# Kernel tuning notes

Hardware: AMD Instinct MI355X
Metric: run time of the kernel (lower is better)

Reference implementation:

```python
import jax, jax.numpy as jnp
import numpy as np

NUM_LAYERS = 3
NODE_DIM = 32
TIME_DIM = 32
N_HEAD = 4
N_NODES = 1_000_000
BATCH = 256
MODEL_DIM = NODE_DIM + TIME_DIM  # 64
HEAD_DIM = MODEL_DIM // N_HEAD   # 16


def setup_inputs() -> dict:
    key = jax.random.key(0)
    ks = jax.random.split(key, 20)
    L, D, F = NUM_LAYERS, MODEL_DIM, NODE_DIM
    s = 0.1
    return {
        "src_idx": jax.random.randint(ks[0], (BATCH,), 0, N_NODES),
        "target_idx": jax.random.randint(ks[1], (BATCH,), 0, N_NODES),
        "cut_time": jax.random.uniform(ks[2], (BATCH,), dtype=jnp.float32) * 10000.0,
        "num_neighbors": 20,
        # learned params
        "emb": jax.random.uniform(ks[3], (N_NODES, F), minval=-1.0, maxval=1.0, dtype=jnp.float32),
        "time_freq": (1.0 / 10.0 ** jnp.linspace(0.0, 9.0, TIME_DIM)).astype(jnp.float32),
        "time_phase": jnp.zeros((TIME_DIM,), jnp.float32),
        "Wq": jax.random.normal(ks[4], (L, D, D), jnp.float32) * s,
        "Wk": jax.random.normal(ks[5], (L, D, D), jnp.float32) * s,
        "Wv": jax.random.normal(ks[6], (L, D, D), jnp.float32) * s,
        "Wo": jax.random.normal(ks[7], (L, D, D), jnp.float32) * s,
        "mw1": jax.random.normal(ks[8], (L, D + F, F), jnp.float32) * s,
        "mb1": jnp.zeros((L, F), jnp.float32),
        "mw2": jax.random.normal(ks[9], (L, F, F), jnp.float32) * s,
        "mb2": jnp.zeros((L, F), jnp.float32),
        "aff_w1": jax.random.normal(ks[10], (2 * F, F), jnp.float32) * s,
        "aff_b1": jnp.zeros((F,), jnp.float32),
        "aff_w2": jax.random.normal(ks[11], (F, 1), jnp.float32) * s,
        "aff_b2": jnp.zeros((1,), jnp.float32),
    }


def _time_encode(ts, freq, phase):
    # ts: [...]; output [..., TIME_DIM] harmonic encoding (TGAT TimeEncode)
    return jnp.cos(ts[..., None] * freq + phase)


def _sample_neighbors(nodes, times, num_neighbors):
    # Deterministic stand-in for ngh_finder.get_temporal_neighbor (CPU sampler).
    j = jnp.arange(num_neighbors)
    ngh = (nodes[:, None] * 101 + (j + 1) * 7919) % N_NODES        # [n, K] int
    frac = (j + 1).astype(times.dtype) / (num_neighbors + 1)
    ngh_t = times[:, None] * frac                                  # earlier timestamps
    return ngh, ngh_t


def _attn_layer(l, src_feat, src_t_emb, ngh_feat, ngh_t_emb, mask, p):
    # TGAT-style AttnModel: MHA over [feat||time_emb], then MergeLayer(attn_out, src_feat)
    n, K = ngh_feat.shape[0], ngh_feat.shape[1]
    q_in = jnp.concatenate([src_feat, src_t_emb], axis=-1)            # [n, D]
    k_in = jnp.concatenate([ngh_feat, ngh_t_emb], axis=-1)           # [n, K, D]
    q = (q_in @ p["Wq"][l]).reshape(n, N_HEAD, HEAD_DIM)
    k = (k_in @ p["Wk"][l]).reshape(n, K, N_HEAD, HEAD_DIM)
    v = (k_in @ p["Wv"][l]).reshape(n, K, N_HEAD, HEAD_DIM)
    scores = jnp.einsum("nhd,nkhd->nhk", q, k) / jnp.sqrt(jnp.float32(HEAD_DIM))
    scores = jnp.where(mask[:, None, :], -1e9, scores)
    attn = jax.nn.softmax(scores, axis=-1)
    out = jnp.einsum("nhk,nkhd->nhd", attn, v).reshape(n, MODEL_DIM) @ p["Wo"][l]
    h = jax.nn.relu(jnp.concatenate([out, src_feat], axis=-1) @ p["mw1"][l] + p["mb1"][l])
    return h @ p["mw2"][l] + p["mb2"][l]                              # [n, F]


def _tem_conv(nodes, times, layer, num_neighbors, p):
    feat = p["emb"][nodes]                                            # gather [n, F]
    if layer == 0:
        return feat
    src_conv = _tem_conv(nodes, times, layer - 1, num_neighbors, p)   # [n, F]
    ngh, ngh_t = _sample_neighbors(nodes, times, num_neighbors)       # [n, K]
    delta = times[:, None] - ngh_t                                    # [n, K]
    n = nodes.shape[0]
    ngh_conv = _tem_conv(ngh.reshape(-1), ngh_t.reshape(-1), layer - 1,
                         num_neighbors, p).reshape(n, num_neighbors, NODE_DIM)
    src_t_emb = _time_encode(jnp.zeros_like(times), p["time_freq"], p["time_phase"])  # [n, T]
    ngh_t_emb = _time_encode(delta, p["time_freq"], p["time_phase"])  # [n, K, T]
    mask = ngh == 0
    return _attn_layer(layer - 1, src_conv, src_t_emb, ngh_conv, ngh_t_emb, mask, p)


def reference(src_idx, target_idx, cut_time, num_neighbors, emb, time_freq, time_phase,
              Wq, Wk, Wv, Wo, mw1, mb1, mw2, mb2, aff_w1, aff_b1, aff_w2, aff_b2):
    p = dict(emb=emb, time_freq=time_freq, time_phase=time_phase, Wq=Wq, Wk=Wk, Wv=Wv,
             Wo=Wo, mw1=mw1, mb1=mb1, mw2=mw2, mb2=mb2)
    src_embed = _tem_conv(src_idx, cut_time, NUM_LAYERS, num_neighbors, p)
    tgt_embed = _tem_conv(target_idx, cut_time, NUM_LAYERS, num_neighbors, p)
    h = jax.nn.relu(jnp.concatenate([src_embed, tgt_embed], axis=-1) @ aff_w1 + aff_b1)
    return (h @ aff_w2 + aff_b2).squeeze(-1)                          # [B]
```

## Files before the change

kernel.cpp:

```cpp
#include <hip/hip_runtime.h>
#include <math.h>

#define K 20
#define KP1 21
#define F 32
#define NNODES 1000000

#define NP1 112896
#define NP2 5376
#define NP3 256

#define WBLK 16640
#define OFF_H1 49920
#define OFF_H2 (OFF_H1 + 2 * NP1 * F)
#define OFF_H3 (OFF_H2 + 2 * NP2 * F)

#define LDS_M4   12544
#define LDS_WAVE 13568
#define WV_STRIDE 3296
#define SMEM_FLOATS (LDS_WAVE + 8 * WV_STRIDE)

__device__ __forceinline__ int nhash(int node, int j) {
    return (node * 101 + (j + 1) * 7919) % NNODES;
}

__global__ __launch_bounds__(256) void transform_weights(
    const float* __restrict__ Wq, const float* __restrict__ Wk,
    const float* __restrict__ Wv, const float* __restrict__ Wo,
    const float* __restrict__ mw1, const float* __restrict__ mw2,
    const float* __restrict__ phase, float* __restrict__ ws)
{
    const int l = blockIdx.x, tid = threadIdx.x;
    const float* wq = Wq + l * 4096; const float* wk = Wk + l * 4096;
    const float* wv = Wv + l * 4096; const float* wo = Wo + l * 4096;
    const float* m1 = mw1 + l * 3072; const float* m2 = mw2 + l * 1024;
    float* out = ws + l * WBLK;
    for (int i = tid; i < 8192; i += 256) {
        const int a = i >> 8, e = (i >> 2) & 63, h = i & 3;
        float s = 0.f;
        for (int t = 0; t < 16; ++t) s += wq[a * 64 + h * 16 + t] * wk[e * 64 + h * 16 + t];
        out[i] = s;
    }
    for (int i = tid; i < 256; i += 256) {
        const int e = i >> 2, h = i & 3;
        float s = 0.f;
        for (int a = 0; a < 32; ++a) {
            float acc = 0.f;
            for (int t = 0; t < 16; ++t) acc += wq[(32 + a) * 64 + h * 16 + t] * wk[e * 64 + h * 16 + t];
            s += cosf(phase[a]) * acc;
        }
        out[8192 + i] = s;
    }
    for (int i = tid; i < 4096; i += 256) {
        const int e4 = i >> 8, d = (i >> 2) & 63, c = i & 3;
        out[8448 + i] = wv[(4 * e4 + c) * 64 + d];
    }
    for (int i = tid; i < 3072; i += 256) {
        const int k4 = i >> 7, f = (i >> 2) & 31, c = i & 3;
        const int k = 4 * k4 + c;
        float v;
        if (k < 64) { v = 0.f; for (int g2 = 0; g2 < 64; ++g2) v += wo[k * 64 + g2] * m1[g2 * 32 + f]; }
        else v = m1[k * 32 + f];
        out[12544 + i] = v;
    }
    for (int i = tid; i < 1024; i += 256) {
        const int e4 = i >> 7, d = (i >> 2) & 31, c = i & 3;
        out[15616 + i] = m2[(4 * e4 + c) * 32 + d];
    }
}

template<int LEVEL>
__global__ __launch_bounds__(512, 2) void attn_kernel(
    const int* __restrict__ src_idx, const int* __restrict__ tgt_idx,
    const float* __restrict__ cut_time, const float* __restrict__ emb,
    const float* __restrict__ freq, const float* __restrict__ phase,
    const float* __restrict__ ws_w,
    const float* __restrict__ mb1_, const float* __restrict__ mb2_,
    const float* __restrict__ h_in, float* __restrict__ h_out)
{
    constexpr int NPAIRS = (LEVEL == 1) ? NP1 : (LEVEL == 2 ? NP2 : NP3);
    constexpr int PREVN  = (LEVEL == 2) ? NP1 : NP2;
    constexpr int l = LEVEL - 1;
    constexpr int NBATCH = NPAIRS;

    extern __shared__ float smem[];

    const int tid  = threadIdx.x;
    const int w    = tid >> 6;
    const int lane = tid & 63;
    const int h    = lane >> 4;
    const int c3   = lane & 7;
    const int rep  = (lane >> 3) & 1;
    const int td   = lane & 31;
    const int half = lane >> 5;

    {
        const float* wsrc = ws_w + l * WBLK;
        for (int i4 = tid; i4 < 3136; i4 += 512)
            *(float4*)&smem[i4 * 4] = *(const float4*)&wsrc[i4 * 4];
        for (int i4 = tid; i4 < 256; i4 += 512)
            *(float4*)&smem[LDS_M4 + i4 * 4] = *(const float4*)&wsrc[15616 + i4 * 4];
    }
    __syncthreads();

    float* sM   = smem;
    float* sC   = smem + 8192;
    float* sWv4 = smem + 8448;
    float* sm4  = smem + LDS_M4;
    float* wb   = smem + LDS_WAVE + w * WV_STRIDE;
    float* kin0 = wb;
    float* kin1 = wb + 1280;
    float* qf0  = wb + 2560;
    float* qf1  = wb + 2592;
    float* qz0  = wb + 2624;
    float* qz1  = wb + 2896;
    float* ob0  = wb + 3168;
    float* ob1  = wb + 3232;

    const float* P4g = ws_w + l * WBLK + 12544;

    const float fr = freq[td], ph = phase[td];
    const float b1v = mb1_[l * 32 + td], b2v = mb2_[l * 32 + td];

    const int gstride = gridDim.x * 8;
    float4 pf[2][3]; int na[2]; float ta[2];

    auto PRE = [&](int bb) {
        #pragma unroll
        for (int q = 0; q < 2; ++q) {
            const int i    = bb * 2 + q;
            const int side = (i >= NPAIRS) ? 1 : 0;
            const int p    = i - side * NPAIRS;
            int b, s2 = 0, r = 0;
            if (LEVEL == 3)      { b = p; }
            else if (LEVEL == 2) { b = p / KP1; s2 = p % KP1; }
            else                 { int qq = p / KP1; r = p % KP1; b = qq / KP1; s2 = qq % KP1; }
            const int root = side ? tgt_idx[b] : src_idx[b];
            const float ct = cut_time[b];
            int nodeA; float tA;
            if (LEVEL == 3) { nodeA = root; tA = ct; }
            else if (LEVEL == 2) {
                nodeA = s2 ? nhash(root, s2 - 1) : root;
                tA    = s2 ? ct * ((float)s2 / 21.0f) : ct;
            } else {
                const int   n2 = s2 ? nhash(root, s2 - 1) : root;
                const float t2 = s2 ? ct * ((float)s2 / 21.0f) : ct;
                nodeA = r ? nhash(n2, r - 1) : n2;
                tA    = r ? t2 * ((float)r / 21.0f) : t2;
            }
            na[q] = nodeA; ta[q] = tA;
            if (LEVEL == 1) {
                { const int row = lane >> 3, c4 = lane & 7;
                  const int node = row ? nhash(nodeA, row - 1) : nodeA;
                  pf[q][0] = *(const float4*)&emb[(size_t)node * F + c4 * 4]; }
                { const int idx4 = 64 + lane, row = idx4 >> 3, c4 = idx4 & 7;
                  const int node = nhash(nodeA, row - 1);
                  pf[q][1] = *(const float4*)&emb[(size_t)node * F + c4 * 4]; }
                { const int idx4 = 128 + lane;
                  if (idx4 < 168) {
                      const int row = idx4 >> 3, c4 = idx4 & 7;
                      const int node = nhash(nodeA, row - 1);
                      pf[q][2] = *(const float4*)&emb[(size_t)node * F + c4 * 4]; } }
            } else {
                const float* base = h_in + ((size_t)side * PREVN + (size_t)p * KP1) * F;
                pf[q][0] = *(const float4*)&base[lane * 4];
                pf[q][1] = *(const float4*)&base[(64 + lane) * 4];
                if (128 + lane < 168) pf[q][2] = *(const float4*)&base[(128 + lane) * 4];
            }
        }
    };

    int g = blockIdx.x * 8 + w;
    if (g < NBATCH) PRE(g);

    for (; g < NBATCH; g += gstride) {
        const int gs = g;
        const int cna0 = na[0], cna1 = na[1];
        const float cta0 = ta[0], cta1 = ta[1];

        #pragma unroll
        for (int q = 0; q < 2; ++q) {
            float* kin = q ? kin1 : kin0;
            float* qfb = q ? qf1 : qf0;
            { const int row = lane >> 3, c4 = lane & 7;
              if (row == 0) *(float4*)&qfb[c4 * 4] = pf[q][0];
              else          *(float4*)&kin[(row - 1) * 64 + c4 * 4] = pf[q][0]; }
            { const int idx4 = 64 + lane, row = idx4 >> 3, c4 = idx4 & 7;
              *(float4*)&kin[(row - 1) * 64 + c4 * 4] = pf[q][1]; }
            { const int idx4 = 128 + lane;
              if (idx4 < 168) { const int row = idx4 >> 3, c4 = idx4 & 7;
                *(float4*)&kin[(row - 1) * 64 + c4 * 4] = pf[q][2]; } }
        }

        #pragma unroll
        for (int it = 0; it < 10; ++it) {
            const int j = it * 2 + half;
            { const float ngh_t = cta0 * ((float)(j + 1) / 21.0f);
              const float delta = cta0 - ngh_t;
              kin0[j * 64 + 32 + td] = cosf(delta * fr + ph); }
            { const float ngh_t = cta1 * ((float)(j + 1) / 21.0f);
              const float delta = cta1 - ngh_t;
              kin1[j * 64 + 32 + td] = cosf(delta * fr + ph); }
        }
        unsigned mb[2];
        { int m = (cna0 * 101 + 7919) % NNODES; unsigned bits = 0;
          #pragma unroll
          for (int j = 0; j < K; ++j) { if (m == 0) bits |= (1u << j); m += 7919; if (m >= NNODES) m -= NNODES; }
          mb[0] = bits; }
        { int m = (cna1 * 101 + 7919) % NNODES; unsigned bits = 0;
          #pragma unroll
          for (int j = 0; j < K; ++j) { if (m == 0) bits |= (1u << j); m += 7919; if (m >= NNODES) m -= NNODES; }
          mb[1] = bits; }

        if (g + gstride < NBATCH) PRE(g + gstride);

        float4 acc0 = *(const float4*)&sC[lane * 4];
        float4 acc1 = acc0;
        #pragma unroll
        for (int a4 = 0; a4 < 8; ++a4) {
            const float4 f0 = *(float4*)&qf0[a4 * 4];
            const float4 f1 = *(float4*)&qf1[a4 * 4];
            const float4 m0 = *(const float4*)&sM[(a4 * 4 + 0) * 256 + lane * 4];
            const float4 m1v = *(const float4*)&sM[(a4 * 4 + 1) * 256 + lane * 4];
            const float4 m2v = *(const float4*)&sM[(a4 * 4 + 2) * 256 + lane * 4];
            const float4 m3 = *(const float4*)&sM[(a4 * 4 + 3) * 256 + lane * 4];
            acc0.x += f0.x * m0.x + f0.y * m1v.x + f0.z * m2v.x + f0.w * m3.x;
            acc0.y += f0.x * m0.y + f0.y * m1v.y + f0.z * m2v.y + f0.w * m3.y;
            acc0.z += f0.x * m0.z + f0.y * m1v.z + f0.z * m2v.z + f0.w * m3.z;
            acc0.w += f0.x * m0.w + f0.y * m1v.w + f0.z * m2v.w + f0.w * m3.w;
            acc1.x += f1.x * m0.x + f1.y * m1v.x + f1.z * m2v.x + f1.w * m3.x;
            acc1.y += f1.x * m0.y + f1.y * m1v.y + f1.z * m2v.y + f1.w * m3.y;
            acc1.z += f1.x * m0.z + f1.y * m1v.z + f1.z * m2v.z + f1.w * m3.z;
            acc1.w += f1.x * m0.w + f1.y * m1v.w + f1.z * m2v.w + f1.w * m3.w;
        }
        qz0[0 * 68 + lane] = acc0.x; qz0[1 * 68 + lane] = acc0.y;
        qz0[2 * 68 + lane] = acc0.z; qz0[3 * 68 + lane] = acc0.w;
        qz1[0 * 68 + lane] = acc1.x; qz1[1 * 68 + lane] = acc1.y;
        qz1[2 * 68 + lane] = acc1.z; qz1[3 * 68 + lane] = acc1.w;

        const int ofsA = c3 * 8 + rep * 4;
        const int ofsB = c3 * 8 + 4 - rep * 4;
        const int j0 = rep * 10;
        #pragma unroll
        for (int q = 0; q < 2; ++q) {
            float* kin = q ? kin1 : kin0;
            float* qzb = q ? qz1 : qz0;
            const float4 qkA = *(float4*)&qzb[h * 68 + ofsA];
            const float4 qkB = *(float4*)&qzb[h * 68 + ofsB];
            float sc[10];
            #pragma unroll
            for (int t = 0; t < 10; ++t) {
                const float4 kA = *(float4*)&kin[(j0 + t) * 64 + ofsA];
                const float4 kB = *(float4*)&kin[(j0 + t) * 64 + ofsB];
                sc[t] = qkA.x * kA.x + qkA.y * kA.y + qkA.z * kA.z + qkA.w * kA.w
                      + qkB.x * kB.x + qkB.y * kB.y + qkB.z * kB.z + qkB.w * kB.w;
            }
            #pragma unroll
            for (int off = 1; off < 8; off <<= 1) {
                #pragma unroll
                for (int t = 0; t < 10; ++t) sc[t] += __shfl_xor(sc[t], off, 8);
            }
            #pragma unroll
            for (int t = 0; t < 10; ++t) {
                float s = sc[t] * 0.25f;
                if ((mb[q] >> (j0 + t)) & 1) s = -1e9f;
                sc[t] = s;
            }
            float mx = sc[0];
            #pragma unroll
            for (int t = 1; t < 10; ++t) mx = fmaxf(mx, sc[t]);
            mx = fmaxf(mx, __shfl_xor(mx, 8, 16));
            float sum = 0.f;
            #pragma unroll
            for (int t = 0; t < 10; ++t) { sc[t] = __expf(sc[t] - mx); sum += sc[t]; }
            sum += __shfl_xor(sum, 8, 16);
            const float inv = 1.0f / sum;
            float4 zA = {0, 0, 0, 0}, zB = {0, 0, 0, 0};
            #pragma unroll
            for (int t = 0; t < 10; ++t) {
                const float4 kA = *(float4*)&kin[(j0 + t) * 64 + ofsA];
                const float4 kB = *(float4*)&kin[(j0 + t) * 64 + ofsB];
                zA.x += sc[t] * kA.x; zA.y += sc[t] * kA.y; zA.z += sc[t] * kA.z; zA.w += sc[t] * kA.w;
                zB.x += sc[t] * kB.x; zB.y += sc[t] * kB.y; zB.z += sc[t] * kB.z; zB.w += sc[t] * kB.w;
            }
            float4 fA, fB;
            fA.x = zA.x + __shfl_xor(zB.x, 8, 16); fA.y = zA.y + __shfl_xor(zB.y, 8, 16);
            fA.z = zA.z + __shfl_xor(zB.z, 8, 16); fA.w = zA.w + __shfl_xor(zB.w, 8, 16);
            fB.x = zB.x + __shfl_xor(zA.x, 8, 16); fB.y = zB.y + __shfl_xor(zA.y, 8, 16);
            fB.z = zB.z + __shfl_xor(zA.z, 8, 16); fB.w = zB.w + __shfl_xor(zA.w, 8, 16);
            fA.x *= inv; fA.y *= inv; fA.z *= inv; fA.w *= inv;
            fB.x *= inv; fB.y *= inv; fB.z *= inv; fB.w *= inv;
            if (rep == 0) {
                *(float4*)&qzb[h * 68 + ofsA] = fA;
                *(float4*)&qzb[h * 68 + ofsB] = fB;
            }
        }

        float od0 = 0.f, od1 = 0.f;
        #pragma unroll
        for (int e4 = 0; e4 < 16; ++e4) {
            const float4 wv = *(float4*)&sWv4[e4 * 256 + lane * 4];
            const float4 z0 = *(float4*)&qz0[h * 68 + e4 * 4];
            const float4 z1 = *(float4*)&qz1[h * 68 + e4 * 4];
            od0 += z0.x * wv.x + z0.y * wv.y + z0.z * wv.z + z0.w * wv.w;
            od1 += z1.x * wv.x + z1.y * wv.y + z1.z * wv.z + z1.w * wv.w;
        }
        ob0[lane] = od0;
        ob1[lane] = od1;

        float hv0 = 0.f, hv1 = 0.f;
        #pragma unroll
        for (int e4 = 0; e4 < 12; ++e4) {
            float4 x0, x1;
            if (half == 0) { x0 = *(float4*)&ob0[e4 * 4]; x1 = *(float4*)&ob1[e4 * 4]; }
            else {
                x0 = (e4 < 4) ? *(float4*)&ob0[48 + e4 * 4] : *(float4*)&qf0[(e4 - 4) * 4];
                x1 = (e4 < 4) ? *(float4*)&ob1[48 + e4 * 4] : *(float4*)&qf1[(e4 - 4) * 4];
            }
            const float4 w4 = *(const float4*)&P4g[(half * 12 + e4) * 128 + td * 4];
            hv0 += x0.x * w4.x + x0.y * w4.y + x0.z * w4.z + x0.w * w4.w;
            hv1 += x1.x * w4.x + x1.y * w4.y + x1.z * w4.z + x1.w * w4.w;
        }
        hv0 += __shfl_xor(hv0, 32);
        hv1 += __shfl_xor(hv1, 32);
        hv0 = fmaxf(hv0 + b1v, 0.0f);
        hv1 = fmaxf(hv1 + b1v, 0.0f);
        if (lane < 32) { ob0[td] = hv0; ob1[td] = hv1; }

        float y0 = 0.f, y1 = 0.f;
        #pragma unroll
        for (int e4 = 0; e4 < 4; ++e4) {
            const float4 w4 = *(float4*)&sm4[(half * 4 + e4) * 128 + td * 4];
            const float4 x0 = *(float4*)&ob0[half * 16 + e4 * 4];
            const float4 x1 = *(float4*)&ob1[half * 16 + e4 * 4];
            y0 += x0.x * w4.x + x0.y * w4.y + x0.z * w4.z + x0.w * w4.w;
            y1 += x1.x * w4.x + x1.y * w4.y + x1.z * w4.z + x1.w * w4.w;
        }
        y0 += __shfl_xor(y0, 32);
        y1 += __shfl_xor(y1, 32);
        if (lane < 32) {
            #pragma unroll
            for (int q = 0; q < 2; ++q) {
                const int i    = gs * 2 + q;
                const int side = (i >= NPAIRS) ? 1 : 0;
                const int p    = i - side * NPAIRS;
                const float y  = (q == 0) ? y0 : y1;
                h_out[((size_t)side * NPAIRS + p) * F + td] = y + b2v;
            }
        }
    }
}

__global__ __launch_bounds__(256) void final_kernel(
    const float* __restrict__ h3,
    const float* __restrict__ aw1, const float* __restrict__ ab1,
    const float* __restrict__ aw2, const float* __restrict__ ab2,
    float* __restrict__ out)
{
    const int bidx = threadIdx.x;
    float x[64];
    #pragma unroll
    for (int e = 0; e < 32; ++e) {
        x[e]      = h3[(size_t)bidx * 32 + e];
        x[32 + e] = h3[((size_t)NP3 + bidx) * 32 + e];
    }
    float acc = ab2[0];
    for (int f = 0; f < 32; ++f) {
        float hv = ab1[f];
        #pragma unroll
        for (int e = 0; e < 64; ++e) hv += x[e] * aw1[e * 32 + f];
        acc += fmaxf(hv, 0.0f) * aw2[f];
    }
    out[bidx] = acc;
}

extern "C" void kernel_launch(void* const* d_in, const int* in_sizes, int n_in,
                              void* d_out, int out_size, void* d_ws, size_t ws_size,
                              hipStream_t stream)
{
    const int*   src_idx = (const int*)d_in[0];
    const int*   tgt_idx = (const int*)d_in[1];
    const float* cut     = (const float*)d_in[2];
    const float* emb   = (const float*)d_in[4];
    const float* freq  = (const float*)d_in[5];
    const float* phase = (const float*)d_in[6];
    const float* Wq    = (const float*)d_in[7];
    const float* Wk    = (const float*)d_in[8];
    const float* Wv    = (const float*)d_in[9];
    const float* Wo    = (const float*)d_in[10];
    const float* mw1   = (const float*)d_in[11];
    const float* mb1   = (const float*)d_in[12];
    const float* mw2   = (const float*)d_in[13];
    const float* mb2   = (const float*)d_in[14];
    const float* aw1   = (const float*)d_in[15];
    const float* ab1   = (const float*)d_in[16];
    const float* aw2   = (const float*)d_in[17];
    const float* ab2   = (const float*)d_in[18];

    float* ws = (float*)d_ws;
    float* h1 = ws + OFF_H1;
    float* h2 = ws + OFF_H2;
    float* h3 = ws + OFF_H3;

    const size_t smem_bytes = SMEM_FLOATS * sizeof(float);
    hipFuncSetAttribute((const void*)attn_kernel<1>, hipFuncAttributeMaxDynamicSharedMemorySize, (int)smem_bytes);
    hipFuncSetAttribute((const void*)attn_kernel<2>, hipFuncAttributeMaxDynamicSharedMemorySize, (int)smem_bytes);
    hipFuncSetAttribute((const void*)attn_kernel<3>, hipFuncAttributeMaxDynamicSharedMemorySize, (int)smem_bytes);

    transform_weights<<<dim3(3), dim3(256), 0, stream>>>(Wq, Wk, Wv, Wo, mw1, mw2, phase, ws);
    attn_kernel<1><<<dim3(256), dim3(512), smem_bytes, stream>>>(
        src_idx, tgt_idx, cut, emb, freq, phase, ws, mb1, mb2, (const float*)nullptr, h1);
    attn_kernel<2><<<dim3(256), dim3(512), smem_bytes, stream>>>(
        src_idx, tgt_idx, cut, emb, freq, phase, ws, mb1, mb2, h1, h2);
    attn_kernel<3><<<dim3(32), dim3(512), smem_bytes, stream>>>(
        src_idx, tgt_idx, cut, emb, freq, phase, ws, mb1, mb2, h2, h3);
    final_kernel<<<dim3(1), dim3(256), 0, stream>>>(h3, aw1, ab1, aw2, ab2, (float*)d_out);
}
```

Baseline: 797.5 us.

## Pair src and tgt sides per wave to share time encodings and drop occupancy hint

```diff
diff --git a/kernel.cpp b/kernel.cpp
--- a/kernel.cpp
+++ b/kernel.cpp
@@ -70,7 +70,7 @@
 }
 
 template<int LEVEL>
-__global__ __launch_bounds__(512, 2) void attn_kernel(
+__global__ __launch_bounds__(512) void attn_kernel(
     const int* __restrict__ src_idx, const int* __restrict__ tgt_idx,
     const float* __restrict__ cut_time, const float* __restrict__ emb,
     const float* __restrict__ freq, const float* __restrict__ phase,
@@ -81,7 +81,6 @@
     constexpr int NPAIRS = (LEVEL == 1) ? NP1 : (LEVEL == 2 ? NP2 : NP3);
     constexpr int PREVN  = (LEVEL == 2) ? NP1 : NP2;
     constexpr int l = LEVEL - 1;
-    constexpr int NBATCH = NPAIRS;
 
     extern __shared__ float smem[];
 
@@ -123,32 +122,33 @@
     const float b1v = mb1_[l * 32 + td], b2v = mb2_[l * 32 + td];
 
     const int gstride = gridDim.x * 8;
-    float4 pf[2][3]; int na[2]; float ta[2];
-
-    auto PRE = [&](int bb) {
+    float4 pf[2][3]; int na[2]; float ta;
+
+    auto PRE = [&](int p) {
+        int b, s2 = 0, r = 0;
+        if (LEVEL == 3)      { b = p; }
+        else if (LEVEL == 2) { b = p / KP1; s2 = p % KP1; }
+        else                 { int qq = p / KP1; r = p % KP1; b = qq / KP1; s2 = qq % KP1; }
+        const float ct = cut_time[b];
+        const int root0 = src_idx[b];
+        const int root1 = tgt_idx[b];
+        if (LEVEL == 3) { ta = ct; }
+        else if (LEVEL == 2) { ta = s2 ? ct * ((float)s2 / 21.0f) : ct; }
+        else {
+            const float t2 = s2 ? ct * ((float)s2 / 21.0f) : ct;
+            ta = r ? t2 * ((float)r / 21.0f) : t2;
+        }
         #pragma unroll
         for (int q = 0; q < 2; ++q) {
-            const int i    = bb * 2 + q;
-            const int side = (i >= NPAIRS) ? 1 : 0;
-            const int p    = i - side * NPAIRS;
-            int b, s2 = 0, r = 0;
-            if (LEVEL == 3)      { b = p; }
-            else if (LEVEL == 2) { b = p / KP1; s2 = p % KP1; }
-            else                 { int qq = p / KP1; r = p % KP1; b = qq / KP1; s2 = qq % KP1; }
-            const int root = side ? tgt_idx[b] : src_idx[b];
-            const float ct = cut_time[b];
-            int nodeA; float tA;
-            if (LEVEL == 3) { nodeA = root; tA = ct; }
-            else if (LEVEL == 2) {
-                nodeA = s2 ? nhash(root, s2 - 1) : root;
-                tA    = s2 ? ct * ((float)s2 / 21.0f) : ct;
-            } else {
-                const int   n2 = s2 ? nhash(root, s2 - 1) : root;
-                const float t2 = s2 ? ct * ((float)s2 / 21.0f) : ct;
+            const int root = q ? root1 : root0;
+            int nodeA;
+            if (LEVEL == 3) { nodeA = root; }
+            else if (LEVEL == 2) { nodeA = s2 ? nhash(root, s2 - 1) : root; }
+            else {
+                const int n2 = s2 ? nhash(root, s2 - 1) : root;
                 nodeA = r ? nhash(n2, r - 1) : n2;
-                tA    = r ? t2 * ((float)r / 21.0f) : t2;
-            }
-            na[q] = nodeA; ta[q] = tA;
+            }
+            na[q] = nodeA;
             if (LEVEL == 1) {
                 { const int row = lane >> 3, c4 = lane & 7;
                   const int node = row ? nhash(nodeA, row - 1) : nodeA;
@@ -162,7 +162,7 @@
                       const int node = nhash(nodeA, row - 1);
                       pf[q][2] = *(const float4*)&emb[(size_t)node * F + c4 * 4]; } }
             } else {
-                const float* base = h_in + ((size_t)side * PREVN + (size_t)p * KP1) * F;
+                const float* base = h_in + ((size_t)q * PREVN + (size_t)p * KP1) * F;
                 pf[q][0] = *(const float4*)&base[lane * 4];
                 pf[q][1] = *(const float4*)&base[(64 + lane) * 4];
                 if (128 + lane < 168) pf[q][2] = *(const float4*)&base[(128 + lane) * 4];
@@ -171,12 +171,12 @@
     };
 
     int g = blockIdx.x * 8 + w;
-    if (g < NBATCH) PRE(g);
-
-    for (; g < NBATCH; g += gstride) {
+    if (g < NPAIRS) PRE(g);
+
+    for (; g < NPAIRS; g += gstride) {
         const int gs = g;
         const int cna0 = na[0], cna1 = na[1];
-        const float cta0 = ta[0], cta1 = ta[1];
+        const float cta = ta;
 
         #pragma unroll
         for (int q = 0; q < 2; ++q) {
@@ -195,12 +195,11 @@
         #pragma unroll
         for (int it = 0; it < 10; ++it) {
             const int j = it * 2 + half;
-            { const float ngh_t = cta0 * ((float)(j + 1) / 21.0f);
-              const float delta = cta0 - ngh_t;
-              kin0[j * 64 + 32 + td] = cosf(delta * fr + ph); }
-            { const float ngh_t = cta1 * ((float)(j + 1) / 21.0f);
-              const float delta = cta1 - ngh_t;
-              kin1[j * 64 + 32 + td] = cosf(delta * fr + ph); }
+            const float ngh_t = cta * ((float)(j + 1) / 21.0f);
+            const float delta = cta - ngh_t;
+            const float cv = cosf(delta * fr + ph);
+            kin0[j * 64 + 32 + td] = cv;
+            kin1[j * 64 + 32 + td] = cv;
         }
         unsigned mb[2];
         { int m = (cna0 * 101 + 7919) % NNODES; unsigned bits = 0;
@@ -212,7 +211,7 @@
           for (int j = 0; j < K; ++j) { if (m == 0) bits |= (1u << j); m += 7919; if (m >= NNODES) m -= NNODES; }
           mb[1] = bits; }
 
-        if (g + gstride < NBATCH) PRE(g + gstride);
+        if (g + gstride < NPAIRS) PRE(g + gstride);
 
         float4 acc0 = *(const float4*)&sC[lane * 4];
         float4 acc1 = acc0;
@@ -339,14 +338,8 @@
         y0 += __shfl_xor(y0, 32);
         y1 += __shfl_xor(y1, 32);
         if (lane < 32) {
-            #pragma unroll
-            for (int q = 0; q < 2; ++q) {
-                const int i    = gs * 2 + q;
-                const int side = (i >= NPAIRS) ? 1 : 0;
-                const int p    = i - side * NPAIRS;
-                const float y  = (q == 0) ? y0 : y1;
-                h_out[((size_t)side * NPAIRS + p) * F + td] = y + b2v;
-            }
+            h_out[((size_t)0 * NPAIRS + gs) * F + td] = y0 + b2v;
+            h_out[((size_t)1 * NPAIRS + gs) * F + td] = y1 + b2v;
         }
     }
 }
```

After: 725.8 us. -9.0%, faster.
